# Kernel optimization log

Hardware: AMD Instinct MI355X
Metric: run time of the kernel (lower is better)

The kernel has to match this reference:

```python
import jax, jax.numpy as jnp
import numpy as np

EPS = 1e-08

def setup_inputs() -> dict:
    key = jax.random.key(0)
    k1, k2, k3, k4 = jax.random.split(key, 4)
    B, T, D, D_sample = 16, 512, 2048, 4096
    z_hist = jax.random.normal(k1, (B, T, D), dtype=jnp.float32)
    decay_rates = jax.random.normal(k2, (D_sample,), dtype=jnp.float32)
    idx_i = jax.random.randint(k3, (D_sample,), 0, D)
    idx_j = jax.random.randint(k4, (D_sample,), 0, D)
    return {"z_hist": z_hist, "decay_rates": decay_rates, "idx_i": idx_i, "idx_j": idx_j}

def reference(z_hist, decay_rates, idx_i, idx_j):
    B, T, D = z_hist.shape
    r = jax.nn.softplus(decay_rates)                      # [N]
    times = jnp.arange(T, dtype=z_hist.dtype)             # [T]
    # decay[t, n] = exp(-r_n * (T - 1 - t))
    decay = jnp.exp(-r[None, :] * (T - 1 - times)[:, None])  # [T, N]
    z_i = z_hist[:, :, idx_i]                              # [B, T, N]
    z_j = z_hist[:, :, idx_j]                              # [B, T, N]
    num = jnp.einsum('btn,btn,tn->bn', z_i, z_j, decay)    # [B, N]
    den = jnp.sqrt(decay.sum(axis=0) + EPS)                # [N]
    return num / den[None, :]
```

## Files before the change

kernel.cpp:

```cpp
#include <hip/hip_runtime.h>
#include <math.h>

#define B_    16
#define T_    512
#define D_    2048
#define DS_   4096
#define TCHUNK 4
#define TCPB   2
#define TSPLIT (T_ / (TCHUNK * TCPB))
#define EPS_  1e-8f
#define CLOG  34.5f


__device__ __forceinline__ float softplus_f(float x) {
    return (x > 20.f) ? x : log1pf(expf(x));
}

__global__ __launch_bounds__(256) void pre_kernel(const float* __restrict__ decay_rates,
                                                  float* __restrict__ num,
                                                  float* __restrict__ inv_den) {
    int gtid = blockIdx.x * 256 + threadIdx.x;
    num[gtid] = 0.f;
    if (gtid < DS_) {
        float r = softplus_f(decay_rates[gtid]);
        float S = expm1f(-r * (float)T_) / expm1f(-r);
        inv_den[gtid] = 1.0f / sqrtf(S + EPS_);
    }
}

__global__ __launch_bounds__(1024) void sort_kernel(const float* __restrict__ decay_rates,
                                                    const int* __restrict__ idx_i,
                                                    const int* __restrict__ idx_j,
                                                    float* __restrict__ g_s,
                                                    float* __restrict__ e4m_s,
                                                    float* __restrict__ nr_s,
                                                    int* __restrict__ pair_s,
                                                    int* __restrict__ nout_s,
                                                    int* __restrict__ hcap_s) {
    __shared__ int hist[64];
    const int tid = threadIdx.x;
    if (tid < 64) hist[tid] = 0;
    __syncthreads();
    #pragma unroll
    for (int k = 0; k < 4; ++k) {
        int n = tid + k * 1024;
        float r = softplus_f(decay_rates[n]);
        float hf = CLOG / r;
        int h = (hf >= 511.f) ? 511 : (int)hf;
        atomicAdd(&hist[h >> 3], 1);
    }
    __syncthreads();
    if (tid == 0) {
        int run = 0;
        for (int q = 63; q >= 0; --q) { int c = hist[q]; hist[q] = run; run += c; }
    }
    __syncthreads();
    #pragma unroll
    for (int k = 0; k < 4; ++k) {
        int n = tid + k * 1024;
        float r = softplus_f(decay_rates[n]);
        float hf = CLOG / r;
        int h = (hf >= 511.f) ? 511 : (int)hf;
        int q = h >> 3;
        int pos = atomicAdd(&hist[q], 1);
        g_s[pos]    = expf(r);
        e4m_s[pos]  = expf(-4.f * r);
        nr_s[pos]   = -r;
        pair_s[pos] = idx_i[n] | (idx_j[n] << 16);
        nout_s[pos] = n;
        hcap_s[pos] = (q << 3) | 7;
    }
}

__global__ __launch_bounds__(256, 4) void main_kernel(const float* __restrict__ z,
                                                      const float* __restrict__ g_s,
                                                      const float* __restrict__ e4m_s,
                                                      const float* __restrict__ nr_s,
                                                      const int* __restrict__ pair_s,
                                                      const int* __restrict__ nout_s,
                                                      const int* __restrict__ hcap_s,
                                                      float* __restrict__ num) {
    __shared__ float4 quads[D_];
    const int tbase = blockIdx.x * (TCHUNK * TCPB);
    const int b     = blockIdx.y;
    const int tid   = threadIdx.x;

    int hb[16];
    #pragma unroll
    for (int s = 0; s < 16; ++s)
        hb[s] = __builtin_amdgcn_readfirstlane(hcap_s[tid + s * 256]);

    const int kbW = 504 - tbase;
    const int kb1 = 507 - tbase;

    float g[16], w0[16], acc[16];
    int pair[16];
    #pragma unroll
    for (int s = 0; s < 16; ++s) {
        acc[s] = 0.f;
        if (hb[s] >= kbW) {
            int m = tid + s * 256;
            pair[s] = pair_s[m];
            g[s]    = g_s[m];
            w0[s]   = __expf(nr_s[m] * (float)kb1);
        }
    }

    const float* zb = z + (size_t)b * T_ * D_;
    #pragma unroll 1
    for (int c = TCPB - 1; c >= 0; --c) {
        const int t0 = tbase + c * TCHUNK;
        const float* base = zb + (size_t)t0 * D_;
        #pragma unroll
        for (int it = 0; it < D_ / 256; ++it) {
            int ci = tid + it * 256;
            quads[ci] = make_float4(base[ci], base[D_ + ci],
                                    base[2 * D_ + ci], base[3 * D_ + ci]);
        }
        __syncthreads();
        const int kmin = 508 - t0;
        #pragma unroll
        for (int s = 0; s < 16; ++s) {
            if (hb[s] >= kmin) {
                int pk = pair[s];
                float4 vi = quads[pk & 0xFFFF];
                float4 vj = quads[pk >> 16];
                float gs = g[s];
                float h3 = vi.w * vj.w;
                float h2 = fmaf(h3, gs, vi.z * vj.z);
                float h1 = fmaf(h2, gs, vi.y * vj.y);
                float h0 = fmaf(h1, gs, vi.x * vj.x);
                acc[s] = fmaf(w0[s], h0, acc[s]);
                if (c > 0) w0[s] *= e4m_s[tid + s * 256];
            }
        }
        __syncthreads();
    }
    #pragma unroll
    for (int s = 0; s < 16; ++s)
        if (hb[s] >= kbW && acc[s] != 0.f)
            atomicAdd(&num[b * DS_ + nout_s[tid + s * 256]], acc[s]);
}

__global__ __launch_bounds__(256) void fin_kernel(const float* __restrict__ num,
                                                  const float* __restrict__ inv_den,
                                                  float* __restrict__ out) {
    int gtid = blockIdx.x * 256 + threadIdx.x;
    out[gtid] = num[gtid] * inv_den[gtid & (DS_ - 1)];
}

extern "C" void kernel_launch(void* const* d_in, const int* in_sizes, int n_in,
                              void* d_out, int out_size, void* d_ws, size_t ws_size,
                              hipStream_t stream) {
    const float* z  = (const float*)d_in[0];
    const float* dr = (const float*)d_in[1];
    const int*   ii = (const int*)d_in[2];
    const int*   jj = (const int*)d_in[3];
    float* out = (float*)d_out;

    float* num     = (float*)d_ws;
    float* inv_den = num + B_ * DS_;
    float* g_s     = inv_den + DS_;
    float* e4m_s   = g_s + DS_;
    float* nr_s    = e4m_s + DS_;
    int*   pair_s  = (int*)(nr_s + DS_);
    int*   nout_s  = pair_s + DS_;
    int*   hcap_s  = nout_s + DS_;

    hipLaunchKernelGGL(pre_kernel, dim3((B_ * DS_) / 256), dim3(256), 0, stream,
                       dr, num, inv_den);
    hipLaunchKernelGGL(sort_kernel, dim3(1), dim3(1024), 0, stream,
                       dr, ii, jj, g_s, e4m_s, nr_s, pair_s, nout_s, hcap_s);
    hipLaunchKernelGGL(main_kernel, dim3(TSPLIT, B_), dim3(256), 0, stream,
                       z, g_s, e4m_s, nr_s, pair_s, nout_s, hcap_s, num);
    hipLaunchKernelGGL(fin_kernel, dim3((B_ * DS_) / 256), dim3(256), 0, stream,
                       num, inv_den, out);
}
```

Before: 150.3 us.

## Replace atomics with per-timegroup partial sums and async global-to-LDS row loads

The main kernel now processes one 4-timestep group per block and loads rows straight into LDS with global_load_lds, dropping the float4 transpose and the two-chunk loop. Instead of atomically adding into num, each block writes its partial result to a large [TG, B, DS] buffer. The final kernel then reduces only the relevant time groups per sorted pair and scatters to output order. This removes the atomics, the num zeroing and the e4m table, but it adds a much larger workspace and a strided reduction pass with more global traffic.

After: 151.7 us. About the same (+0.9%).

```diff
diff --git a/kernel.cpp b/kernel.cpp
--- a/kernel.cpp
+++ b/kernel.cpp
@@ -5,9 +5,8 @@
 #define T_    512
 #define D_    2048
 #define DS_   4096
-#define TCHUNK 4
-#define TCPB   2
-#define TSPLIT (T_ / (TCHUNK * TCPB))
+#define TG_   128
+#define RS_   2052
 #define EPS_  1e-8f
 #define CLOG  34.5f
 
@@ -16,23 +15,24 @@
     return (x > 20.f) ? x : log1pf(expf(x));
 }
 
+__device__ __forceinline__ void glds16(const float* g, float* l) {
+    __builtin_amdgcn_global_load_lds((const __attribute__((address_space(1))) void*)g,
+                                     (__attribute__((address_space(3))) void*)l,
+                                     16, 0, 0);
+}
+
 __global__ __launch_bounds__(256) void pre_kernel(const float* __restrict__ decay_rates,
-                                                  float* __restrict__ num,
                                                   float* __restrict__ inv_den) {
-    int gtid = blockIdx.x * 256 + threadIdx.x;
-    num[gtid] = 0.f;
-    if (gtid < DS_) {
-        float r = softplus_f(decay_rates[gtid]);
-        float S = expm1f(-r * (float)T_) / expm1f(-r);
-        inv_den[gtid] = 1.0f / sqrtf(S + EPS_);
-    }
+    int n = blockIdx.x * 256 + threadIdx.x;
+    float r = softplus_f(decay_rates[n]);
+    float S = expm1f(-r * (float)T_) / expm1f(-r);
+    inv_den[n] = 1.0f / sqrtf(S + EPS_);
 }
 
 __global__ __launch_bounds__(1024) void sort_kernel(const float* __restrict__ decay_rates,
                                                     const int* __restrict__ idx_i,
                                                     const int* __restrict__ idx_j,
                                                     float* __restrict__ g_s,
-                                                    float* __restrict__ e4m_s,
                                                     float* __restrict__ nr_s,
                                                     int* __restrict__ pair_s,
                                                     int* __restrict__ nout_s,
@@ -64,7 +64,6 @@
         int q = h >> 3;
         int pos = atomicAdd(&hist[q], 1);
         g_s[pos]    = expf(r);
-        e4m_s[pos]  = expf(-4.f * r);
         nr_s[pos]   = -r;
         pair_s[pos] = idx_i[n] | (idx_j[n] << 16);
         nout_s[pos] = n;
@@ -72,81 +71,78 @@
     }
 }
 
-__global__ __launch_bounds__(256, 4) void main_kernel(const float* __restrict__ z,
-                                                      const float* __restrict__ g_s,
-                                                      const float* __restrict__ e4m_s,
-                                                      const float* __restrict__ nr_s,
-                                                      const int* __restrict__ pair_s,
-                                                      const int* __restrict__ nout_s,
-                                                      const int* __restrict__ hcap_s,
-                                                      float* __restrict__ num) {
-    __shared__ float4 quads[D_];
-    const int tbase = blockIdx.x * (TCHUNK * TCPB);
-    const int b     = blockIdx.y;
-    const int tid   = threadIdx.x;
+__global__ __launch_bounds__(256) void main_kernel(const float* __restrict__ z,
+                                                   const float* __restrict__ g_s,
+                                                   const float* __restrict__ nr_s,
+                                                   const int* __restrict__ pair_s,
+                                                   const int* __restrict__ hcap_s,
+                                                   float* __restrict__ num) {
+    __shared__ float rows[4 * RS_];
+    const int tg   = blockIdx.x;
+    const int b    = blockIdx.y;
+    const int tid  = threadIdx.x;
+    const int wave = tid >> 6, lane = tid & 63;
+    const int tb   = tg * 4;
+    const int kminB = 508 - tb;
+    const int kb0   = 511 - tb;
 
-    int hb[16];
+    const float* src = z + ((size_t)b * T_ + tb + wave) * D_ + lane * 4;
+    float* dst = rows + wave * RS_;
     #pragma unroll
-    for (int s = 0; s < 16; ++s)
-        hb[s] = __builtin_amdgcn_readfirstlane(hcap_s[tid + s * 256]);
+    for (int s = 0; s < 8; ++s)
+        glds16(src + s * 256, dst + s * 256);
 
-    const int kbW = 504 - tbase;
-    const int kb1 = 507 - tbase;
-
-    float g[16], w0[16], acc[16];
-    int pair[16];
+    int hcv[16];
+    #pragma unroll
+    for (int s = 0; s < 16; ++s) hcv[s] = hcap_s[tid + s * 256];
+    int hb[16], pair[16]; float g[16], w0[16];
     #pragma unroll
     for (int s = 0; s < 16; ++s) {
-        acc[s] = 0.f;
-        if (hb[s] >= kbW) {
+        hb[s] = __builtin_amdgcn_readfirstlane(hcv[s]);
+        if (hb[s] >= kminB) {
             int m = tid + s * 256;
             pair[s] = pair_s[m];
             g[s]    = g_s[m];
-            w0[s]   = __expf(nr_s[m] * (float)kb1);
+            w0[s]   = __expf(nr_s[m] * (float)kb0);
         }
     }
 
-    const float* zb = z + (size_t)b * T_ * D_;
-    #pragma unroll 1
-    for (int c = TCPB - 1; c >= 0; --c) {
-        const int t0 = tbase + c * TCHUNK;
-        const float* base = zb + (size_t)t0 * D_;
-        #pragma unroll
-        for (int it = 0; it < D_ / 256; ++it) {
-            int ci = tid + it * 256;
-            quads[ci] = make_float4(base[ci], base[D_ + ci],
-                                    base[2 * D_ + ci], base[3 * D_ + ci]);
+    asm volatile("s_waitcnt vmcnt(0)" ::: "memory");
+    __syncthreads();
+
+    #pragma unroll
+    for (int s = 0; s < 16; ++s) {
+        if (hb[s] >= kminB) {
+            int ci = pair[s] & 0xFFFF, cj = pair[s] >> 16;
+            float vi0 = rows[ci],           vj0 = rows[cj];
+            float vi1 = rows[RS_ + ci],     vj1 = rows[RS_ + cj];
+            float vi2 = rows[2 * RS_ + ci], vj2 = rows[2 * RS_ + cj];
+            float vi3 = rows[3 * RS_ + ci], vj3 = rows[3 * RS_ + cj];
+            float gs = g[s];
+            float h3 = vi3 * vj3;
+            float h2 = fmaf(h3, gs, vi2 * vj2);
+            float h1 = fmaf(h2, gs, vi1 * vj1);
+            float h0 = fmaf(h1, gs, vi0 * vj0);
+            num[((size_t)tg * B_ + b) * DS_ + tid + s * 256] = w0[s] * h0;
         }
-        __syncthreads();
-        const int kmin = 508 - t0;
-        #pragma unroll
-        for (int s = 0; s < 16; ++s) {
-            if (hb[s] >= kmin) {
-                int pk = pair[s];
-                float4 vi = quads[pk & 0xFFFF];
-                float4 vj = quads[pk >> 16];
-                float gs = g[s];
-                float h3 = vi.w * vj.w;
-                float h2 = fmaf(h3, gs, vi.z * vj.z);
-                float h1 = fmaf(h2, gs, vi.y * vj.y);
-                float h0 = fmaf(h1, gs, vi.x * vj.x);
-                acc[s] = fmaf(w0[s], h0, acc[s]);
-                if (c > 0) w0[s] *= e4m_s[tid + s * 256];
-            }
-        }
-        __syncthreads();
     }
-    #pragma unroll
-    for (int s = 0; s < 16; ++s)
-        if (hb[s] >= kbW && acc[s] != 0.f)
-            atomicAdd(&num[b * DS_ + nout_s[tid + s * 256]], acc[s]);
 }
 
 __global__ __launch_bounds__(256) void fin_kernel(const float* __restrict__ num,
                                                   const float* __restrict__ inv_den,
+                                                  const int* __restrict__ nout_s,
+                                                  const int* __restrict__ hcap_s,
                                                   float* __restrict__ out) {
-    int gtid = blockIdx.x * 256 + threadIdx.x;
-    out[gtid] = num[gtid] * inv_den[gtid & (DS_ - 1)];
+    int gt = blockIdx.x * 256 + threadIdx.x;
+    int m  = gt & (DS_ - 1);
+    int b  = gt >> 12;
+    int hc = hcap_s[(m >> 6) << 6];
+    int tgmin = (511 - hc) >> 2; if (tgmin < 0) tgmin = 0;
+    float sum = 0.f;
+    for (int tg = tgmin; tg < TG_; ++tg)
+        sum += num[((size_t)tg * B_ + b) * DS_ + m];
+    int n = nout_s[m];
+    out[b * DS_ + n] = sum * inv_den[n];
 }
 
 extern "C" void kernel_launch(void* const* d_in, const int* in_sizes, int n_in,
@@ -159,20 +155,18 @@
     float* out = (float*)d_out;
 
     float* num     = (float*)d_ws;
-    float* inv_den = num + B_ * DS_;
+    float* inv_den = num + (size_t)TG_ * B_ * DS_;
     float* g_s     = inv_den + DS_;
-    float* e4m_s   = g_s + DS_;
-    float* nr_s    = e4m_s + DS_;
+    float* nr_s    = g_s + DS_;
     int*   pair_s  = (int*)(nr_s + DS_);
     int*   nout_s  = pair_s + DS_;
     int*   hcap_s  = nout_s + DS_;
 
-    hipLaunchKernelGGL(pre_kernel, dim3((B_ * DS_) / 256), dim3(256), 0, stream,
-                       dr, num, inv_den);
+    hipLaunchKernelGGL(pre_kernel, dim3(DS_ / 256), dim3(256), 0, stream, dr, inv_den);
     hipLaunchKernelGGL(sort_kernel, dim3(1), dim3(1024), 0, stream,
-                       dr, ii, jj, g_s, e4m_s, nr_s, pair_s, nout_s, hcap_s);
-    hipLaunchKernelGGL(main_kernel, dim3(TSPLIT, B_), dim3(256), 0, stream,
-                       z, g_s, e4m_s, nr_s, pair_s, nout_s, hcap_s, num);
+                       dr, ii, jj, g_s, nr_s, pair_s, nout_s, hcap_s);
+    hipLaunchKernelGGL(main_kernel, dim3(TG_, B_), dim3(256), 0, stream,
+                       z, g_s, nr_s, pair_s, hcap_s, num);
     hipLaunchKernelGGL(fin_kernel, dim3((B_ * DS_) / 256), dim3(256), 0, stream,
-                       num, inv_den, out);
+                       num, inv_den, nout_s, hcap_s, out);
 }
```
